# Performance work log

Measured on AMD Instinct MI355X. Metric: run time of the kernel, lower is better.

## Reference

```python
import jax, jax.numpy as jnp
import numpy as np

B, N, F = 4, 4096, 6
N_CENTROIDS, NSAMPLES, RADIUS = 1024, 64, 0.2


def fps(coords, n_c):
    # iterative farthest point sampling, vectorized over batch
    Bb, Nn, _ = coords.shape
    batch = jnp.arange(Bb)
    first = jnp.zeros((Bb,), jnp.int32)
    init_dist = jnp.full((Bb, Nn), 1e9, coords.dtype)

    def step(carry, _):
        dist, last = carry
        p = coords[batch, last]                      # (B,3) last chosen point
        d = jnp.sum((coords - p[:, None, :]) ** 2, -1)
        dist = jnp.minimum(dist, d)
        nxt = jnp.argmax(dist, -1).astype(jnp.int32)
        return (dist, nxt), nxt

    _, rest = jax.lax.scan(step, (init_dist, first), None, length=n_c - 1)
    return jnp.concatenate([first[None, :], rest], 0).T  # (B, n_c)


def ball_query(coords, centroids, radius, s):
    # coords (B,N,3), centroids (B,C,3) -> (B,C,S) neighbor indices
    Nn = coords.shape[1]
    d = jnp.sum((centroids[:, :, None, :] - coords[:, None, :, :]) ** 2, -1)  # (B,C,N)
    idx = jnp.where(d > radius * radius, Nn, jnp.arange(Nn))
    idx = jnp.sort(idx, axis=-1)[..., :s]
    first = idx[..., :1]                              # centroid itself always valid
    return jnp.where(idx == Nn, first, idx)


def tnet(h, w1, w2, w3, f1, f2):
    # h: (B, P, ch) -> (B, ch, ch) transform matrix (T-Net)
    ch = h.shape[-1]
    t = jax.nn.relu(h @ w1)
    t = jax.nn.relu(t @ w2)
    t = jax.nn.relu(t @ w3)
    t = t.max(axis=1)                                 # global max pool over points
    t = jax.nn.relu(t @ f1)
    return (t @ f2).reshape(-1, ch, ch) + jnp.eye(ch, dtype=h.dtype)


def setup_inputs() -> dict:
    key = jax.random.key(0)
    ks = jax.random.split(key, 20)
    sc = 0.02
    p = lambda k, shape: sc * jax.random.normal(k, shape, dtype=jnp.float32)
    return {
        'x': jax.random.normal(ks[0], (B, N, F), dtype=jnp.float32),
        'points': jax.random.uniform(ks[1], (B, N, 3), dtype=jnp.float32),
        # input T-Net (F x F)
        't1_w1': p(ks[2], (F, 64)), 't1_w2': p(ks[3], (64, 128)), 't1_w3': p(ks[4], (128, 256)),
        't1_f1': p(ks[5], (256, 128)), 't1_f2': p(ks[6], (128, F * F)),
        't2_w1': p(ks[7], (64, 64)), 't2_w2': p(ks[8], (64, 128)), 't2_w3': p(ks[9], (128, 256)),
        't2_f1': p(ks[10], (256, 128)), 't2_f2': p(ks[11], (128, 64 * 64)),
        # shared MLP
        'w1': p(ks[12], (F, 64)), 'w2': p(ks[13], (64, 128)), 'w3': p(ks[14], (128, 256)),
    }


def reference(x, points, t1_w1, t1_w2, t1_w3, t1_f1, t1_f2,
              t2_w1, t2_w2, t2_w3, t2_f1, t2_f2, w1, w2, w3):
    idx = fps(points, N_CENTROIDS)                                       # (B,C)
    centroids = jnp.take_along_axis(points, idx[..., None], axis=1)      # (B,C,3)
    gidx = ball_query(points, centroids, RADIUS, NSAMPLES)               # (B,C,S)
    gather = jax.vmap(lambda a, i: a[i])
    g_xyz = gather(points, gidx) - centroids[:, :, None, :]              # (B,C,S,3)
    g_feat = gather(x, gidx)                                             # (B,C,S,F)

    flat = g_feat.reshape(g_feat.shape[0], -1, g_feat.shape[-1])         # (B,C*S,F)
    inT = tnet(flat, t1_w1, t1_w2, t1_w3, t1_f1, t1_f2)                  # (B,F,F)
    h = jnp.einsum('bpc,bcd->bpd', flat, inT)
    h = jax.nn.relu(h @ w1)                                              # (B,C*S,64)
    feT = tnet(h, t2_w1, t2_w2, t2_w3, t2_f1, t2_f2)                     # (B,64,64)
    h = jnp.einsum('bpc,bcd->bpd', h, feT)
    h = jax.nn.relu(h @ w2)
    h = jax.nn.relu(h @ w3)                                              # (B,C*S,256)
    feats = h.reshape(h.shape[0], N_CENTROIDS, NSAMPLES, -1).max(axis=2) # (B,C,256)
    feats = feats.transpose(0, 2, 1)                                     # (B,256,C)
    return centroids, g_xyz.transpose(0, 3, 1, 2), feats, inT, feT
```

## Files before the change

kernel.cpp:

```cpp
#include <hip/hip_runtime.h>

#define Bb 4
#define Np 4096
#define Ff 6
#define NC 1024
#define NSAMP 64
#define NPTS (Bb*Np)
#define R2 ((float)(0.2*0.2))

static __host__ __device__ constexpr size_t alup(size_t x){ return (x + 255) & ~(size_t)255; }
static constexpr size_t OFF_GIDX = 0;
static constexpr size_t SZ_GIDX  = (size_t)Bb*NC*NSAMP*4;
static constexpr size_t OFF_MASK = alup(OFF_GIDX + SZ_GIDX);
static constexpr size_t SZ_MASK  = (size_t)Bb*Np*4;
static constexpr size_t OFF_T1   = OFF_MASK + SZ_MASK;
static constexpr size_t OFF_T2   = OFF_T1 + (size_t)Bb*256*4;
static constexpr size_t ZERO_BYTES = (OFF_T2 + (size_t)Bb*256*4) - OFF_MASK;
static constexpr size_t OFF_INT  = alup(OFF_T2 + (size_t)Bb*256*4);
static constexpr size_t OFF_FET  = alup(OFF_INT + (size_t)Bb*36*4);
static constexpr size_t OFF_XT    = alup(OFF_FET + (size_t)Bb*4096*4);
static constexpr size_t OFF_HW    = alup(OFF_XT + (size_t)6*NPTS*4);
static constexpr size_t OFF_BUF64 = alup(OFF_HW + (size_t)64*NPTS*4);
static constexpr size_t OFF_BUF128= alup(OFF_BUF64 + (size_t)64*NPTS*4);
static constexpr size_t OFF_FINAL = alup(OFF_BUF128 + (size_t)128*NPTS*4);

__device__ __forceinline__ unsigned wave_red_umax(unsigned v)
{
#define DPP_STEP(ctrl) { unsigned t = (unsigned)__builtin_amdgcn_update_dpp((int)v, (int)v, ctrl, 0xF, 0xF, false); v = (t > v) ? t : v; }
    DPP_STEP(0x111)
    DPP_STEP(0x112)
    DPP_STEP(0x114)
    DPP_STEP(0x118)
    DPP_STEP(0x142)
    DPP_STEP(0x143)
#undef DPP_STEP
    return v;
}

template<int CTRL>
__device__ __forceinline__ double dpp_max_f64(double v)
{
    int lo = __double2loint(v), hi = __double2hiint(v);
    int tlo = __builtin_amdgcn_update_dpp(lo, lo, CTRL, 0xF, 0xF, false);
    int thi = __builtin_amdgcn_update_dpp(hi, hi, CTRL, 0xF, 0xF, false);
    return fmax(v, __hiloint2double(thi, tlo));
}

__global__ __launch_bounds__(256) void fps_kernel(const float* __restrict__ points,
                                                  float* __restrict__ out_cent,
                                                  const float* __restrict__ x,
                                                  float* __restrict__ xT)
{
    if (blockIdx.x >= Bb) {
        int id = (blockIdx.x - Bb) * 256 + threadIdx.x;
        if (id < Ff * NPTS) {
            int ch = id >> 14;
            int g  = id & (NPTS-1);
            xT[id] = x[(size_t)g * Ff + ch];
        }
        return;
    }

    int b = blockIdx.x;
    const float* P = points + (size_t)b * Np * 3;
    int tid  = threadIdx.x;
    int lane = tid & 63;
    int wave = tid >> 6;

    __shared__ float4 sc[Np];
    __shared__ __align__(16) double swin[2][4];

    float px[16], py[16], pz[16], dist[16];
    int ilo[16];
#pragma unroll
    for (int j = 0; j < 16; ++j) {
        int p = tid + (j << 8);
        float xx = P[p*3+0], yy = P[p*3+1], zz = P[p*3+2];
        px[j] = xx; py[j] = yy; pz[j] = zz;
        dist[j] = 1000000000.0f;
        ilo[j] = ~p;
        sc[p] = make_float4(xx, yy, zz, 0.f);
    }
    __syncthreads();

    float cx = sc[0].x, cy = sc[0].y, cz = sc[0].z;
    if (tid == 0) {
        out_cent[((size_t)b*NC + 0)*3 + 0] = cx;
        out_cent[((size_t)b*NC + 0)*3 + 1] = cy;
        out_cent[((size_t)b*NC + 0)*3 + 2] = cz;
    }

    for (int s = 1; s < NC; ++s) {
        double k0 = -1.0, k1 = -1.0, k2 = -1.0, k3 = -1.0;
#pragma unroll
        for (int j = 0; j < 16; ++j) {
            float dx = __fsub_rn(px[j], cx);
            float dy = __fsub_rn(py[j], cy);
            float dz = __fsub_rn(pz[j], cz);
            float d  = __fadd_rn(__fadd_rn(__fmul_rn(dx,dx), __fmul_rn(dy,dy)), __fmul_rn(dz,dz));
            float nd = fminf(dist[j], d);
            dist[j] = nd;
            double kj = __hiloint2double(__float_as_int(nd), ilo[j]);
            if      ((j & 3) == 0) k0 = fmax(k0, kj);
            else if ((j & 3) == 1) k1 = fmax(k1, kj);
            else if ((j & 3) == 2) k2 = fmax(k2, kj);
            else                   k3 = fmax(k3, kj);
        }
        double key = fmax(fmax(k0, k1), fmax(k2, k3));
        key = dpp_max_f64<0x111>(key);
        key = dpp_max_f64<0x112>(key);
        key = dpp_max_f64<0x114>(key);
        key = dpp_max_f64<0x118>(key);
        key = dpp_max_f64<0x142>(key);
        key = dpp_max_f64<0x143>(key);
        if (lane == 63) swin[s & 1][wave] = key;
        __syncthreads();

        const double2* sw = (const double2*)&swin[s & 1][0];
        double2 p01 = sw[0], p23 = sw[1];
        double kk = fmax(fmax(p01.x, p01.y), fmax(p23.x, p23.y));
        int widx = ~__double2loint(kk);

        float4 c = sc[widx];
        cx = c.x; cy = c.y; cz = c.z;
        if (tid == 0) {
            out_cent[((size_t)b*NC + s)*3 + 0] = cx;
            out_cent[((size_t)b*NC + s)*3 + 1] = cy;
            out_cent[((size_t)b*NC + s)*3 + 2] = cz;
        }
    }
}

__global__ __launch_bounds__(256) void ballq_kernel(const float* __restrict__ points,
                                                    const float* __restrict__ cent,
                                                    int* __restrict__ gidx,
                                                    int* __restrict__ mask,
                                                    float* __restrict__ out_gxyz)
{
    int gtid = blockIdx.x * 256 + threadIdx.x;
    int wid  = gtid >> 6;
    int lane = threadIdx.x & 63;
    int b = wid >> 10, c = wid & 1023;
    const float* P = points + (size_t)b * Np * 3;
    float cx = cent[((size_t)b*NC + c)*3 + 0];
    float cy = cent[((size_t)b*NC + c)*3 + 1];
    float cz = cent[((size_t)b*NC + c)*3 + 2];

    __shared__ int sidx[4][NSAMP];
    int* my = sidx[threadIdx.x >> 6];

    int count = 0;
    for (int base = 0; base < Np; base += 64) {
        int p = base + lane;
        float dx = __fsub_rn(cx, P[p*3+0]);
        float dy = __fsub_rn(cy, P[p*3+1]);
        float dz = __fsub_rn(cz, P[p*3+2]);
        float d  = __fadd_rn(__fadd_rn(__fmul_rn(dx,dx), __fmul_rn(dy,dy)), __fmul_rn(dz,dz));
        bool inr = !(d > R2);
        unsigned long long mball = __ballot(inr);
        int before = __popcll(mball & ((1ull << lane) - 1ull));
        int pos = count + before;
        if (inr && pos < NSAMP) my[pos] = p;
        count += (int)__popcll(mball);
        if (count >= NSAMP) break;
    }
    __syncthreads();
    int total = count < NSAMP ? count : NSAMP;
    int first = my[0];
    int myi = (lane < total) ? my[lane] : first;
    gidx[(size_t)wid * NSAMP + lane] = myi;
    mask[(size_t)b * Np + myi] = 1;
    float qx = P[myi*3+0], qy = P[myi*3+1], qz = P[myi*3+2];
    out_gxyz[(((size_t)b*3 + 0)*NC + c)*NSAMP + lane] = __fsub_rn(qx, cx);
    out_gxyz[(((size_t)b*3 + 1)*NC + c)*NSAMP + lane] = __fsub_rn(qy, cy);
    out_gxyz[(((size_t)b*3 + 2)*NC + c)*NSAMP + lane] = __fsub_rn(qz, cz);
}

template<int K, int N, int NT, bool RELU, bool PM, bool BW, bool TM>
__global__ __launch_bounds__(256) void layer2_k(const float* __restrict__ in,
                                                const float* __restrict__ W,
                                                float* __restrict__ out,
                                                const int* __restrict__ mask,
                                                unsigned* __restrict__ tmax)
{
    static_assert(NT % 4 == 0, "NT multiple of 4");
    int tid = threadIdx.x;
    int g0  = blockIdx.x * 1024 + tid;
    int o0  = blockIdx.y * NT;
    const float* Wb = W;
    if (BW) Wb += (size_t)(blockIdx.x >> 2) * K * N;

    __shared__ __align__(16) float ws[K * NT];
    for (int i = tid; i < K * NT; i += 256)
        ws[i] = Wb[(size_t)(i / NT) * N + o0 + (i % NT)];
    __syncthreads();

    float acc[4][NT];
#pragma unroll
    for (int mi = 0; mi < 4; ++mi)
#pragma unroll
        for (int oo = 0; oo < NT; ++oo) acc[mi][oo] = 0.f;

#pragma unroll 2
    for (int k = 0; k < K; ++k) {
        float a0 = in[(size_t)k * NPTS + g0];
        float a1 = in[(size_t)k * NPTS + g0 + 256];
        float a2 = in[(size_t)k * NPTS + g0 + 512];
        float a3 = in[(size_t)k * NPTS + g0 + 768];
        const float4* wr = (const float4*)&ws[k * NT];
#pragma unroll
        for (int q = 0; q < NT/4; ++q) {
            float4 w = wr[q];
            acc[0][4*q+0] += a0 * w.x;  acc[0][4*q+1] += a0 * w.y;
            acc[0][4*q+2] += a0 * w.z;  acc[0][4*q+3] += a0 * w.w;
            acc[1][4*q+0] += a1 * w.x;  acc[1][4*q+1] += a1 * w.y;
            acc[1][4*q+2] += a1 * w.z;  acc[1][4*q+3] += a1 * w.w;
            acc[2][4*q+0] += a2 * w.x;  acc[2][4*q+1] += a2 * w.y;
            acc[2][4*q+2] += a2 * w.z;  acc[2][4*q+3] += a2 * w.w;
            acc[3][4*q+0] += a3 * w.x;  acc[3][4*q+1] += a3 * w.y;
            acc[3][4*q+2] += a3 * w.z;  acc[3][4*q+3] += a3 * w.w;
        }
    }

    if (TM) {
        float tmv[NT];
#pragma unroll
        for (int oo = 0; oo < NT; ++oo) tmv[oo] = 0.f;
#pragma unroll
        for (int mi = 0; mi < 4; ++mi) {
            bool pres = mask[g0 + mi * 256] != 0;
#pragma unroll
            for (int oo = 0; oo < NT; ++oo) {
                float v = pres ? fmaxf(acc[mi][oo], 0.f) : 0.f;
                tmv[oo] = fmaxf(tmv[oo], v);
            }
        }
        int b = g0 >> 12;
        int lane = tid & 63;
#pragma unroll
        for (int oo = 0; oo < NT; ++oo) {
            unsigned r = wave_red_umax(__float_as_uint(tmv[oo]));
            if (lane == 63)
                atomicMax(&tmax[(b << 8) + o0 + oo], r);
        }
        return;
    }

#pragma unroll
    for (int mi = 0; mi < 4; ++mi) {
        int g = g0 + mi * 256;
#pragma unroll
        for (int oo = 0; oo < NT; ++oo) {
            float v = acc[mi][oo];
            if (RELU) v = fmaxf(v, 0.f);
            if (PM) out[(size_t)g * N + o0 + oo] = v;
            else    out[(size_t)(o0 + oo) * NPTS + g] = v;
        }
    }
}

__global__ __launch_bounds__(256) void l_h_kernel(const float* __restrict__ xT,
                                                  const float* __restrict__ inT,
                                                  const float* __restrict__ w1,
                                                  float* __restrict__ hw)
{
    int g = blockIdx.x * 256 + threadIdx.x;
    int b = g >> 12;
    float v[6];
#pragma unroll
    for (int c = 0; c < 6; ++c) v[c] = xT[(size_t)c * NPTS + g];
    float t[6];
#pragma unroll
    for (int o = 0; o < 6; ++o) {
        float acc = 0.f;
#pragma unroll
        for (int c = 0; c < 6; ++c) acc += v[c] * inT[b*36 + c*6 + o];
        t[o] = acc;
    }
#pragma unroll 8
    for (int j = 0; j < 64; ++j) {
        float acc = 0.f;
#pragma unroll
        for (int o = 0; o < 6; ++o) acc += t[o] * w1[o*64 + j];
        hw[(size_t)j * NPTS + g] = fmaxf(acc, 0.f);
    }
}

__global__ __launch_bounds__(256) void head1_kernel(const float* __restrict__ t1,
                                                    const float* __restrict__ f1,
                                                    const float* __restrict__ f2,
                                                    float* __restrict__ outT, float* __restrict__ wsT)
{
    int b = blockIdx.x, t = threadIdx.x;
    __shared__ float tv[256], u[128];
    tv[t] = t1[(size_t)b*256 + t];
    __syncthreads();
    if (t < 128) {
        float acc = 0.f;
        for (int k = 0; k < 256; ++k) acc += tv[k] * f1[(size_t)k*128 + t];
        u[t] = fmaxf(acc, 0.f);
    }
    __syncthreads();
    if (t < 36) {
        float acc = 0.f;
        for (int k = 0; k < 128; ++k) acc += u[k] * f2[(size_t)k*36 + t];
        if (t / 6 == t % 6) acc += 1.0f;
        outT[b*36 + t] = acc;
        wsT[b*36 + t]  = acc;
    }
}

__global__ __launch_bounds__(256) void head2_kernel(const float* __restrict__ t2,
                                                    const float* __restrict__ f1,
                                                    const float* __restrict__ f2,
                                                    float* __restrict__ outT, float* __restrict__ wsT)
{
    int b = blockIdx.x, t = threadIdx.x;
    __shared__ float tv[256], u[128];
    tv[t] = t2[(size_t)b*256 + t];
    __syncthreads();
    if (t < 128) {
        float acc = 0.f;
        for (int k = 0; k < 256; ++k) acc += tv[k] * f1[(size_t)k*128 + t];
        u[t] = fmaxf(acc, 0.f);
    }
    __syncthreads();
    int j = blockIdx.y * 256 + t;
    float acc = 0.f;
#pragma unroll 8
    for (int k = 0; k < 128; ++k) acc += u[k] * f2[(size_t)k*4096 + j];
    if (j / 64 == j % 64) acc += 1.0f;
    outT[(size_t)b*4096 + j] = acc;
    wsT[(size_t)b*4096 + j]  = acc;
}

__global__ __launch_bounds__(256) void feats_kernel(const float* __restrict__ fin,
                                                    const int* __restrict__ gidx,
                                                    float* __restrict__ out)
{
    int bid = blockIdx.x;
    int b = bid >> 10, c = bid & 1023;
    int o = threadIdx.x;
    __shared__ int sid[NSAMP];
    if (o < NSAMP) sid[o] = gidx[(size_t)bid * NSAMP + o];
    __syncthreads();
    const float* fb = fin + (size_t)b * Np * 256;
    float m = -1e30f;
    for (int s = 0; s < NSAMP; ++s)
        m = fmaxf(m, fb[(size_t)sid[s] * 256 + o]);
    out[((size_t)b*256 + o)*NC + c] = m;
}

extern "C" void kernel_launch(void* const* d_in, const int* in_sizes, int n_in,
                              void* d_out, int out_size, void* d_ws, size_t ws_size,
                              hipStream_t stream)
{
    const float* x      = (const float*)d_in[0];
    const float* points = (const float*)d_in[1];
    const float* t1_w1  = (const float*)d_in[2];
    const float* t1_w2  = (const float*)d_in[3];
    const float* t1_w3  = (const float*)d_in[4];
    const float* t1_f1  = (const float*)d_in[5];
    const float* t1_f2  = (const float*)d_in[6];
    const float* t2_w1  = (const float*)d_in[7];
    const float* t2_w2  = (const float*)d_in[8];
    const float* t2_w3  = (const float*)d_in[9];
    const float* t2_f1  = (const float*)d_in[10];
    const float* t2_f2  = (const float*)d_in[11];
    const float* w1     = (const float*)d_in[12];
    const float* w2     = (const float*)d_in[13];
    const float* w3     = (const float*)d_in[14];

    float* out = (float*)d_out;
    float* out_cent  = out;
    float* out_gxyz  = out + 12288;
    float* out_feats = out + 798720;
    float* out_inT   = out + 1847296;
    float* out_feT   = out + 1847440;

    char* ws = (char*)d_ws;
    int*      gidx  = (int*)(ws + OFF_GIDX);
    int*      mask  = (int*)(ws + OFF_MASK);
    unsigned* t1max = (unsigned*)(ws + OFF_T1);
    unsigned* t2max = (unsigned*)(ws + OFF_T2);
    float*    wsInT = (float*)(ws + OFF_INT);
    float*    wsFeT = (float*)(ws + OFF_FET);
    float*    xT    = (float*)(ws + OFF_XT);
    float*    hw    = (float*)(ws + OFF_HW);
    float*    buf64 = (float*)(ws + OFF_BUF64);
    float*    buf128= (float*)(ws + OFF_BUF128);
    float*    fin   = (float*)(ws + OFF_FINAL);

    (void)hipMemsetAsync(ws + OFF_MASK, 0, ZERO_BYTES, stream);

    fps_kernel<<<Bb + (Ff*NPTS + 255)/256, 256, 0, stream>>>(points, out_cent, x, xT);
    ballq_kernel<<<(Bb*NC)/4, 256, 0, stream>>>(points, out_cent, gidx, mask, out_gxyz);

    layer2_k<6,  64, 16, true,  false, false, false><<<dim3(16, 4), 256, 0, stream>>>(xT,    t1_w1, buf64,  nullptr, nullptr);
    layer2_k<64, 128,16, true,  false, false, false><<<dim3(16, 8), 256, 0, stream>>>(buf64, t1_w2, buf128, nullptr, nullptr);
    layer2_k<128,256,16, false, false, false, true ><<<dim3(16,16), 256, 0, stream>>>(buf128,t1_w3, nullptr, mask, t1max);
    head1_kernel<<<Bb, 256, 0, stream>>>((const float*)t1max, t1_f1, t1_f2, out_inT, wsInT);
    l_h_kernel<<<NPTS/256, 256, 0, stream>>>(xT, wsInT, w1, hw);
    layer2_k<64, 64, 16, true,  false, false, false><<<dim3(16, 4), 256, 0, stream>>>(hw,    t2_w1, buf64,  nullptr, nullptr);
    layer2_k<64, 128,16, true,  false, false, false><<<dim3(16, 8), 256, 0, stream>>>(buf64, t2_w2, buf128, nullptr, nullptr);
    layer2_k<128,256,16, false, false, false, true ><<<dim3(16,16), 256, 0, stream>>>(buf128,t2_w3, nullptr, mask, t2max);
    head2_kernel<<<dim3(Bb,16), 256, 0, stream>>>((const float*)t2max, t2_f1, t2_f2, out_feT, wsFeT);
    layer2_k<64, 64, 16, false, false, true,  false><<<dim3(16, 4), 256, 0, stream>>>(hw,    wsFeT, buf64,  nullptr, nullptr);
    layer2_k<64, 128,16, true,  false, false, false><<<dim3(16, 8), 256, 0, stream>>>(buf64, w2,    buf128, nullptr, nullptr);
    layer2_k<128,256,16, true,  true,  false, false><<<dim3(16,16), 256, 0, stream>>>(buf128,w3,    fin,    nullptr, nullptr);
    feats_kernel<<<Bb*NC, 256, 0, stream>>>(fin, gidx, out_feats);

    (void)in_sizes; (void)n_in; (void)out_size; (void)ws_size;
}
```

Baseline: 791.1 us.

## Overlap input T-Net MLP with FPS in one mega kernel, fuse head into l_h

Moves the first T-Net's three pointwise layers into extra blocks of the FPS launch, so they run on idle CUs alongside the serial FPS loop, and writes pre-activation layer-3 output for all points. A new maxmask kernel then takes the masked ReLU max per channel afterwards, because the mask depends on ball query. The head1 MLP is folded into l_h_kernel, which is recomputed per block, and that kernel reads x directly instead of a transposed copy. FPS now runs with 512 threads and 8 points per thread, which shortens each thread's per-step work but adds more waves to the cross-wave reduction.

```diff
diff --git a/kernel.cpp b/kernel.cpp
--- a/kernel.cpp
+++ b/kernel.cpp
@@ -46,17 +46,94 @@
     return fmax(v, __hiloint2double(thi, tlo));
 }
 
-__global__ __launch_bounds__(256) void fps_kernel(const float* __restrict__ points,
-                                                  float* __restrict__ out_cent,
-                                                  const float* __restrict__ x,
-                                                  float* __restrict__ xT)
-{
+static constexpr int SMEM_BYTES = 84992;
+
+__global__ __launch_bounds__(512) void mega_kernel(const float* __restrict__ points,
+                                                   float* __restrict__ out_cent,
+                                                   const float* __restrict__ x,
+                                                   float* __restrict__ l3pre,
+                                                   const float* __restrict__ t1w1,
+                                                   const float* __restrict__ t1w2,
+                                                   const float* __restrict__ t1w3)
+{
+    __shared__ __align__(16) char smem[SMEM_BYTES];
+
     if (blockIdx.x >= Bb) {
-        int id = (blockIdx.x - Bb) * 256 + threadIdx.x;
-        if (id < Ff * NPTS) {
-            int ch = id >> 14;
-            int g  = id & (NPTS-1);
-            xT[id] = x[(size_t)g * Ff + ch];
+        int tb = blockIdx.x - Bb;
+        int g0 = tb * 64;
+        int t  = threadIdx.x;
+        float* s_in  = (float*)(smem);
+        float* s_w1  = (float*)(smem + 1536);
+        float* s_a1  = (float*)(smem + 3072);
+        float* s_wst = (float*)(smem + 19456);
+        float* s_a2  = (float*)(smem + 52224);
+
+        for (int i = t; i < 384; i += 512) {
+            int pt = i / 6, c = i % 6;
+            s_in[c * 64 + pt] = x[(size_t)(g0 + pt) * 6 + c];
+        }
+        for (int i = t; i < 384; i += 512)  s_w1[i]  = t1w1[i];
+        for (int i = t; i < 8192; i += 512) s_wst[i] = t1w2[i];
+        __syncthreads();
+
+        int pt = t & 63;
+        {
+            int c8 = (t >> 6) * 8;
+            float a[8];
+#pragma unroll
+            for (int i = 0; i < 8; ++i) a[i] = 0.f;
+#pragma unroll
+            for (int k = 0; k < 6; ++k) {
+                float av = s_in[k * 64 + pt];
+#pragma unroll
+                for (int i = 0; i < 8; ++i) a[i] += av * s_w1[k * 64 + c8 + i];
+            }
+#pragma unroll
+            for (int i = 0; i < 8; ++i) s_a1[(c8 + i) * 64 + pt] = fmaxf(a[i], 0.f);
+        }
+        __syncthreads();
+        {
+            int cg = (t >> 6) * 16;
+            float a[16];
+#pragma unroll
+            for (int i = 0; i < 16; ++i) a[i] = 0.f;
+#pragma unroll 4
+            for (int k = 0; k < 64; ++k) {
+                float av = s_a1[k * 64 + pt];
+                const float4* w = (const float4*)&s_wst[k * 128 + cg];
+#pragma unroll
+                for (int q = 0; q < 4; ++q) {
+                    float4 wv = w[q];
+                    a[4*q+0] += av * wv.x; a[4*q+1] += av * wv.y;
+                    a[4*q+2] += av * wv.z; a[4*q+3] += av * wv.w;
+                }
+            }
+#pragma unroll
+            for (int i = 0; i < 16; ++i) s_a2[(cg + i) * 64 + pt] = fmaxf(a[i], 0.f);
+        }
+        __syncthreads();
+        for (int ch0 = 0; ch0 < 256; ch0 += 64) {
+            for (int i = t; i < 8192; i += 512)
+                s_wst[i] = t1w3[((size_t)(i >> 6) << 8) + ch0 + (i & 63)];
+            __syncthreads();
+            int cs = (t >> 6) * 8;
+            float a[8];
+#pragma unroll
+            for (int i = 0; i < 8; ++i) a[i] = 0.f;
+#pragma unroll 4
+            for (int k = 0; k < 128; ++k) {
+                float av = s_a2[k * 64 + pt];
+                const float4* w = (const float4*)&s_wst[k * 64 + cs];
+                float4 w0 = w[0], w1v = w[1];
+                a[0] += av * w0.x;  a[1] += av * w0.y;
+                a[2] += av * w0.z;  a[3] += av * w0.w;
+                a[4] += av * w1v.x; a[5] += av * w1v.y;
+                a[6] += av * w1v.z; a[7] += av * w1v.w;
+            }
+#pragma unroll
+            for (int i = 0; i < 8; ++i)
+                l3pre[(size_t)(ch0 + cs + i) * NPTS + g0 + pt] = a[i];
+            __syncthreads();
         }
         return;
     }
@@ -67,14 +144,14 @@
     int lane = tid & 63;
     int wave = tid >> 6;
 
-    __shared__ float4 sc[Np];
-    __shared__ __align__(16) double swin[2][4];
-
-    float px[16], py[16], pz[16], dist[16];
-    int ilo[16];
-#pragma unroll
-    for (int j = 0; j < 16; ++j) {
-        int p = tid + (j << 8);
+    float4* sc   = (float4*)(smem);
+    double* swin = (double*)(smem + 65536);
+
+    float px[8], py[8], pz[8], dist[8];
+    int ilo[8];
+#pragma unroll
+    for (int j = 0; j < 8; ++j) {
+        int p = tid + (j << 9);
         float xx = P[p*3+0], yy = P[p*3+1], zz = P[p*3+2];
         px[j] = xx; py[j] = yy; pz[j] = zz;
         dist[j] = 1000000000.0f;
@@ -93,7 +170,7 @@
     for (int s = 1; s < NC; ++s) {
         double k0 = -1.0, k1 = -1.0, k2 = -1.0, k3 = -1.0;
 #pragma unroll
-        for (int j = 0; j < 16; ++j) {
+        for (int j = 0; j < 8; ++j) {
             float dx = __fsub_rn(px[j], cx);
             float dy = __fsub_rn(py[j], cy);
             float dz = __fsub_rn(pz[j], cz);
@@ -113,12 +190,13 @@
         key = dpp_max_f64<0x118>(key);
         key = dpp_max_f64<0x142>(key);
         key = dpp_max_f64<0x143>(key);
-        if (lane == 63) swin[s & 1][wave] = key;
+        if (lane == 63) swin[(s & 1) * 8 + wave] = key;
         __syncthreads();
 
-        const double2* sw = (const double2*)&swin[s & 1][0];
-        double2 p01 = sw[0], p23 = sw[1];
-        double kk = fmax(fmax(p01.x, p01.y), fmax(p23.x, p23.y));
+        const double2* sw = (const double2*)&swin[(s & 1) * 8];
+        double2 p01 = sw[0], p23 = sw[1], p45 = sw[2], p67 = sw[3];
+        double kk = fmax(fmax(fmax(p01.x, p01.y), fmax(p23.x, p23.y)),
+                         fmax(fmax(p45.x, p45.y), fmax(p67.x, p67.y)));
         int widx = ~__double2loint(kk);
 
         float4 c = sc[widx];
@@ -176,6 +254,34 @@
     out_gxyz[(((size_t)b*3 + 2)*NC + c)*NSAMP + lane] = __fsub_rn(qz, cz);
 }
 
+__global__ __launch_bounds__(256) void maxmask_kernel(const float* __restrict__ buf,
+                                                      const int* __restrict__ mask,
+                                                      float* __restrict__ tmax)
+{
+    int bid = blockIdx.x;
+    int b = bid >> 8, ch = bid & 255;
+    int tid = threadIdx.x;
+    const float* row = buf + (size_t)ch * NPTS + (size_t)b * Np;
+    const int* mk = mask + (size_t)b * Np;
+    float m = 0.f;
+#pragma unroll
+    for (int i = 0; i < Np / 256; ++i) {
+        int p = tid + i * 256;
+        float v = row[p];
+        if (mk[p]) m = fmaxf(m, fmaxf(v, 0.f));
+    }
+#pragma unroll
+    for (int off = 1; off < 64; off <<= 1)
+        m = fmaxf(m, __shfl_xor(m, off));
+    __shared__ float red[4];
+    if ((tid & 63) == 0) red[tid >> 6] = m;
+    __syncthreads();
+    if (tid == 0) {
+        float r = fmaxf(fmaxf(red[0], red[1]), fmaxf(red[2], red[3]));
+        tmax[(size_t)b * 256 + ch] = r;
+    }
+}
+
 template<int K, int N, int NT, bool RELU, bool PM, bool BW, bool TM>
 __global__ __launch_bounds__(256) void layer2_k(const float* __restrict__ in,
                                                 const float* __restrict__ W,
@@ -259,41 +365,18 @@
     }
 }
 
-__global__ __launch_bounds__(256) void l_h_kernel(const float* __restrict__ xT,
-                                                  const float* __restrict__ inT,
+__global__ __launch_bounds__(256) void l_h_kernel(const float* __restrict__ x,
+                                                  const float* __restrict__ t1max,
+                                                  const float* __restrict__ f1,
+                                                  const float* __restrict__ f2,
                                                   const float* __restrict__ w1,
+                                                  float* __restrict__ out_inT,
                                                   float* __restrict__ hw)
 {
-    int g = blockIdx.x * 256 + threadIdx.x;
-    int b = g >> 12;
-    float v[6];
-#pragma unroll
-    for (int c = 0; c < 6; ++c) v[c] = xT[(size_t)c * NPTS + g];
-    float t[6];
-#pragma unroll
-    for (int o = 0; o < 6; ++o) {
-        float acc = 0.f;
-#pragma unroll
-        for (int c = 0; c < 6; ++c) acc += v[c] * inT[b*36 + c*6 + o];
-        t[o] = acc;
-    }
-#pragma unroll 8
-    for (int j = 0; j < 64; ++j) {
-        float acc = 0.f;
-#pragma unroll
-        for (int o = 0; o < 6; ++o) acc += t[o] * w1[o*64 + j];
-        hw[(size_t)j * NPTS + g] = fmaxf(acc, 0.f);
-    }
-}
-
-__global__ __launch_bounds__(256) void head1_kernel(const float* __restrict__ t1,
-                                                    const float* __restrict__ f1,
-                                                    const float* __restrict__ f2,
-                                                    float* __restrict__ outT, float* __restrict__ wsT)
-{
-    int b = blockIdx.x, t = threadIdx.x;
-    __shared__ float tv[256], u[128];
-    tv[t] = t1[(size_t)b*256 + t];
+    int blk = blockIdx.x, t = threadIdx.x;
+    int b = blk >> 4;
+    __shared__ float tv[256], u[128], sT[36];
+    tv[t] = t1max[(size_t)b*256 + t];
     __syncthreads();
     if (t < 128) {
         float acc = 0.f;
@@ -305,8 +388,29 @@
         float acc = 0.f;
         for (int k = 0; k < 128; ++k) acc += u[k] * f2[(size_t)k*36 + t];
         if (t / 6 == t % 6) acc += 1.0f;
-        outT[b*36 + t] = acc;
-        wsT[b*36 + t]  = acc;
+        sT[t] = acc;
+        if ((blk & 15) == 0) out_inT[b*36 + t] = acc;
+    }
+    __syncthreads();
+
+    int g = blk * 256 + t;
+    float v[6];
+#pragma unroll
+    for (int c = 0; c < 6; ++c) v[c] = x[(size_t)g * 6 + c];
+    float tt[6];
+#pragma unroll
+    for (int o = 0; o < 6; ++o) {
+        float acc = 0.f;
+#pragma unroll
+        for (int c = 0; c < 6; ++c) acc += v[c] * sT[c*6 + o];
+        tt[o] = acc;
+    }
+#pragma unroll 8
+    for (int j = 0; j < 64; ++j) {
+        float acc = 0.f;
+#pragma unroll
+        for (int o = 0; o < 6; ++o) acc += tt[o] * w1[o*64 + j];
+        hw[(size_t)j * NPTS + g] = fmaxf(acc, 0.f);
     }
 }
 
@@ -381,11 +485,9 @@
     char* ws = (char*)d_ws;
     int*      gidx  = (int*)(ws + OFF_GIDX);
     int*      mask  = (int*)(ws + OFF_MASK);
-    unsigned* t1max = (unsigned*)(ws + OFF_T1);
+    float*    t1max = (float*)(ws + OFF_T1);
     unsigned* t2max = (unsigned*)(ws + OFF_T2);
-    float*    wsInT = (float*)(ws + OFF_INT);
     float*    wsFeT = (float*)(ws + OFF_FET);
-    float*    xT    = (float*)(ws + OFF_XT);
     float*    hw    = (float*)(ws + OFF_HW);
     float*    buf64 = (float*)(ws + OFF_BUF64);
     float*    buf128= (float*)(ws + OFF_BUF128);
@@ -393,14 +495,10 @@
 
     (void)hipMemsetAsync(ws + OFF_MASK, 0, ZERO_BYTES, stream);
 
-    fps_kernel<<<Bb + (Ff*NPTS + 255)/256, 256, 0, stream>>>(points, out_cent, x, xT);
+    mega_kernel<<<Bb + 256, 512, 0, stream>>>(points, out_cent, x, fin, t1_w1, t1_w2, t1_w3);
     ballq_kernel<<<(Bb*NC)/4, 256, 0, stream>>>(points, out_cent, gidx, mask, out_gxyz);
-
-    layer2_k<6,  64, 16, true,  false, false, false><<<dim3(16, 4), 256, 0, stream>>>(xT,    t1_w1, buf64,  nullptr, nullptr);
-    layer2_k<64, 128,16, true,  false, false, false><<<dim3(16, 8), 256, 0, stream>>>(buf64, t1_w2, buf128, nullptr, nullptr);
-    layer2_k<128,256,16, false, false, false, true ><<<dim3(16,16), 256, 0, stream>>>(buf128,t1_w3, nullptr, mask, t1max);
-    head1_kernel<<<Bb, 256, 0, stream>>>((const float*)t1max, t1_f1, t1_f2, out_inT, wsInT);
-    l_h_kernel<<<NPTS/256, 256, 0, stream>>>(xT, wsInT, w1, hw);
+    maxmask_kernel<<<Bb*256, 256, 0, stream>>>(fin, mask, t1max);
+    l_h_kernel<<<NPTS/256, 256, 0, stream>>>(x, t1max, t1_f1, t1_f2, w1, out_inT, hw);
     layer2_k<64, 64, 16, true,  false, false, false><<<dim3(16, 4), 256, 0, stream>>>(hw,    t2_w1, buf64,  nullptr, nullptr);
     layer2_k<64, 128,16, true,  false, false, false><<<dim3(16, 8), 256, 0, stream>>>(buf64, t2_w2, buf128, nullptr, nullptr);
     layer2_k<128,256,16, false, false, false, true ><<<dim3(16,16), 256, 0, stream>>>(buf128,t2_w3, nullptr, mask, t2max);
```

Result: slower. 809.4 us (+2.3%).
